# Kernel tuning notes

Hardware: AMD Instinct MI355X
Metric: run time of the kernel (lower is better)

## Reference

```python
import jax, jax.numpy as jnp
import numpy as np

B, S, HID, NH, NKV, HD, PS = 4, 1024, 4096, 32, 8, 128, 16
PPS = S // PS            # pages per sequence
NP = B * PPS             # total pages
NNZ = B * S


def _llama31_freqs(head_dim):
    # flashinfer apply_llama31_rope defaults: theta=5e5, scale=8, low=1, high=4, old_ctx=8192
    half = head_dim // 2
    theta, scale, low_ff, high_ff, old_ctx = 500000.0, 8.0, 1.0, 4.0, 8192.0
    freq = 1.0 / (theta ** (jnp.arange(half, dtype=jnp.float32) * 2.0 / head_dim))
    wavelen = 2.0 * jnp.pi / freq
    low_wl, high_wl = old_ctx / low_ff, old_ctx / high_ff
    smooth = (old_ctx / wavelen - low_ff) / (high_ff - low_ff)
    return jnp.where(wavelen < high_wl, freq,
                     jnp.where(wavelen > low_wl, freq / scale,
                               (1.0 - smooth) * freq / scale + smooth * freq))


def _rope(x, pos, freqs):
    # x: [nnz, H, D], non-interleaved (rotate-half) layout
    ang = pos.astype(jnp.float32)[:, None] * freqs[None, :]          # [nnz, D/2]
    cos, sin = jnp.cos(ang)[:, None, :], jnp.sin(ang)[:, None, :]    # [nnz, 1, D/2]
    x1, x2 = jnp.split(x, 2, axis=-1)
    return jnp.concatenate([x1 * cos - x2 * sin, x2 * cos + x1 * sin], axis=-1)


def setup_inputs() -> dict:
    key = jax.random.key(0)
    ks = jax.random.split(key, 6)
    std = 0.02
    return {
        "hidden_states": jax.random.normal(ks[0], (NNZ, HID), jnp.float32),
        "wq": jax.random.normal(ks[1], (NH * HD, HID), jnp.float32) * std,
        "wk": jax.random.normal(ks[2], (NKV * HD, HID), jnp.float32) * std,
        "wv": jax.random.normal(ks[3], (NKV * HD, HID), jnp.float32) * std,
        "wo": jax.random.normal(ks[4], (HID, NH * HD), jnp.float32) * std,
        "kv_cache": jnp.zeros((1, NP, 2, PS, NKV, HD), jnp.float32),
        "position_ids": jnp.tile(jnp.arange(S, dtype=jnp.int32), B),
        "kv_page_indices": jnp.arange(NP, dtype=jnp.int32),
        "kv_page_indptr": jnp.arange(B + 1, dtype=jnp.int32) * PPS,
        "kv_last_page_lens": jnp.full((B,), PS, jnp.int32),
        "qo_indptr": jnp.arange(B + 1, dtype=jnp.int32) * S,
    }


def reference(hidden_states, wq, wk, wv, wo, kv_cache, position_ids,
              kv_page_indices, kv_page_indptr, kv_last_page_lens, qo_indptr):
    nnz = hidden_states.shape[0]
    b = qo_indptr.shape[0] - 1
    s = nnz // b
    # fused QKV projections (nn.Linear stores [out, in])
    q = (hidden_states @ wq.T).reshape(nnz, NH, HD)
    k = (hidden_states @ wk.T).reshape(nnz, NKV, HD)
    v = (hidden_states @ wv.T).reshape(nnz, NKV, HD)
    # inline Llama-3.1 RoPE with per-token position ids
    freqs = _llama31_freqs(HD)
    q = _rope(q, position_ids, freqs)
    k = _rope(k, position_ids, freqs)
    # paged-KV append: scatter k/v into pages at (page_id, slot)
    cache = kv_cache[0]                                   # [NP, 2, PS, NKV, HD]
    ps = cache.shape[2]
    pages = kv_page_indices.reshape(b, -1)                # [B, PPS]
    bidx = jnp.repeat(jnp.arange(b), s)
    pid = pages[bidx, position_ids // ps]
    slot = position_ids % ps
    cache = cache.at[pid, 0, slot].set(k).at[pid, 1, slot].set(v)
    # paged attention: gather per-sequence K/V from pages, causal SDPA with GQA
    flat = pages.reshape(-1)
    kf = cache[flat, 0].reshape(b, s, NKV, HD)
    vf = cache[flat, 1].reshape(b, s, NKV, HD)
    g = NH // NKV
    kr = jnp.repeat(kf, g, axis=2)                        # [B, S, NH, HD]
    vr = jnp.repeat(vf, g, axis=2)
    qb = q.reshape(b, s, NH, HD)
    scale = 1.0 / jnp.sqrt(jnp.float32(HD))
    scores = jnp.einsum('bqhd,bkhd->bhqk', qb, kr) * scale
    mask = jnp.tril(jnp.ones((s, s), bool))
    scores = jnp.where(mask[None, None], scores, jnp.float32(-1e30))
    attn = jax.nn.softmax(scores, axis=-1)
    out = jnp.einsum('bhqk,bkhd->bqhd', attn, vr).reshape(nnz, NH * HD)
    return out @ wo.T
```

## Files before the change

kernel.cpp:

```cpp
#include <hip/hip_runtime.h>

typedef unsigned short u16;
typedef __bf16 bf16x8 __attribute__((ext_vector_type(8)));
typedef float f32x4 __attribute__((ext_vector_type(4)));

__device__ __forceinline__ u16 f2bf(float f) {
  unsigned int u = __float_as_uint(f);
  u += 0x7fffu + ((u >> 16) & 1u);
  return (u16)(u >> 16);
}
__device__ __forceinline__ float bf2f(u16 v) {
  return __uint_as_float(((unsigned int)v) << 16);
}

__device__ __forceinline__ void gl_lds16(const u16* g, u16* l) {
  auto* lp = reinterpret_cast<__attribute__((address_space(3))) unsigned int*>(
      reinterpret_cast<uintptr_t>(l));
  auto* gp = reinterpret_cast<const __attribute__((address_space(1))) unsigned int*>(
      reinterpret_cast<uintptr_t>(g));
  __builtin_amdgcn_global_load_lds(gp, lp, 16, 0, 0);
}

__global__ __launch_bounds__(256) void cvt_kernel(const float* __restrict__ in,
                                                  u16* __restrict__ out, int n4) {
  int i = blockIdx.x * 256 + threadIdx.x;
  if (i >= n4) return;
  float4 v = ((const float4*)in)[i];
  ushort4 o;
  o.x = f2bf(v.x); o.y = f2bf(v.y); o.z = f2bf(v.z); o.w = f2bf(v.w);
  ((ushort4*)out)[i] = o;
}

template <int OUT_BF16>
__global__ __launch_bounds__(256) void gemm_bt(const u16* __restrict__ A,
                                               const u16* __restrict__ B,
                                               void* __restrict__ Cv, int M, int N, int K) {
  __shared__ u16 As[128 * 32];
  __shared__ u16 Bs[128 * 32];
  const int t = threadIdx.x;
  const int lane = t & 63, w = t >> 6;
  const int col = lane & 15, quad = lane >> 4;
  const int m0 = blockIdx.y * 128, n0 = blockIdx.x * 128;

  f32x4 acc[4][4] = {};

  const int r4 = t >> 2;
  const int c8 = (t & 3) * 8;
  const u16* gA0 = A + (size_t)(m0 + r4) * K + c8;
  const u16* gA1 = A + (size_t)(m0 + 64 + r4) * K + c8;
  const u16* gB0 = B + (size_t)(n0 + r4) * K + c8;
  const u16* gB1 = B + (size_t)(n0 + 64 + r4) * K + c8;
  u16* lA0 = As + w * 512;
  u16* lA1 = As + 2048 + w * 512;
  u16* lB0 = Bs + w * 512;
  u16* lB1 = Bs + 2048 + w * 512;

  const int mr = (w & 1) * 64, nr = (w >> 1) * 64;

  for (int k0 = 0; k0 < K; k0 += 32) {
    __syncthreads();
    gl_lds16(gA0 + k0, lA0);
    gl_lds16(gA1 + k0, lA1);
    gl_lds16(gB0 + k0, lB0);
    gl_lds16(gB1 + k0, lB1);
    __syncthreads();

    bf16x8 a[4], b[4];
#pragma unroll
    for (int i = 0; i < 4; i++)
      a[i] = *(const bf16x8*)&As[(mr + i * 16 + col) * 32 + quad * 8];
#pragma unroll
    for (int i = 0; i < 4; i++)
      b[i] = *(const bf16x8*)&Bs[(nr + i * 16 + col) * 32 + quad * 8];
#pragma unroll
    for (int i = 0; i < 4; i++)
#pragma unroll
      for (int j = 0; j < 4; j++)
        acc[i][j] = __builtin_amdgcn_mfma_f32_16x16x32_bf16(a[i], b[j], acc[i][j], 0, 0, 0);
  }

#pragma unroll
  for (int i = 0; i < 4; i++) {
#pragma unroll
    for (int j = 0; j < 4; j++) {
      int mb = m0 + mr + i * 16 + quad * 4;
      int n = n0 + nr + j * 16 + col;
#pragma unroll
      for (int r = 0; r < 4; r++) {
        float v = acc[i][j][r];
        if constexpr (OUT_BF16)
          ((u16*)Cv)[(size_t)(mb + r) * N + n] = f2bf(v);
        else
          ((float*)Cv)[(size_t)(mb + r) * N + n] = v;
      }
    }
  }
}

__global__ __launch_bounds__(256) void transpose_kernel(const u16* __restrict__ in,
                                                        u16* __restrict__ out,
                                                        int in_stride, int out_stride) {
  __shared__ u16 tile[64][72];
  const int t = threadIdx.x;
  const int bm = blockIdx.y;
  const int bn = blockIdx.x;
  const int r = t >> 3, c = (t & 7) * 8;
  const u16* src = in + (size_t)(bm * 64 + r) * in_stride + bn * 64 + c;
  *(uint4*)&tile[r][c] = *(const uint4*)src;
  *(uint4*)&tile[r + 32][c] = *(const uint4*)(src + (size_t)32 * in_stride);
  __syncthreads();
  u16 vals[8];
  u16* dst = out + (size_t)(bn * 64 + r) * out_stride + bm * 64 + c;
#pragma unroll
  for (int i = 0; i < 8; i++) vals[i] = tile[c + i][r];
  *(uint4*)dst = *(uint4*)vals;
#pragma unroll
  for (int i = 0; i < 8; i++) vals[i] = tile[c + i][r + 32];
  *(uint4*)(dst + (size_t)32 * out_stride) = *(uint4*)vals;
}

__global__ __launch_bounds__(256) void rope_kernel(u16* __restrict__ X,
                                                   const int* __restrict__ pos_ids,
                                                   int log2H, int row_stride) {
  int tid = blockIdx.x * 256 + threadIdx.x;
  int i = tid & 63;
  int rest = tid >> 6;
  int h = rest & ((1 << log2H) - 1);
  int token = rest >> log2H;
  float pos = (float)pos_ids[token];
  float fr = __builtin_exp2f(-(float)i * (18.93156856932417f / 64.0f));
  float wl = 6.283185307179586f / fr;
  float f2;
  if (wl < 2048.0f) f2 = fr;
  else if (wl > 8192.0f) f2 = fr * 0.125f;
  else {
    float sm = (8192.0f / wl - 1.0f) * (1.0f / 3.0f);
    f2 = (1.0f - sm) * fr * 0.125f + sm * fr;
  }
  float ang = pos * f2;
  float ss = sinf(ang), cc = cosf(ang);
  size_t base = (size_t)token * row_stride + (size_t)h * 128 + i;
  float x1 = bf2f(X[base]), x2 = bf2f(X[base + 64]);
  X[base] = f2bf(x1 * cc - x2 * ss);
  X[base + 64] = f2bf(x2 * cc + x1 * ss);
}

__global__ __launch_bounds__(256) void attn_kernel(const u16* __restrict__ Qg,
                                                   const u16* __restrict__ Kg,
                                                   const u16* __restrict__ VTg,
                                                   u16* __restrict__ Og,
                                                   int QS, int KS) {
  const int qt = 15 - blockIdx.x;
  const int h = blockIdx.y, b = blockIdx.z;
  const int kvh = h >> 2;
  const int t = threadIdx.x, lane = t & 63, w = t >> 6;
  const int col = lane & 15, quad = lane >> 4;

  __shared__ u16 Ks[64 * 128];
  __shared__ u16 Vt[128 * 64];
  __shared__ u16 Ps[4][16][72];

  {
    const u16* Qbase = Qg + (size_t)(b * 1024 + qt * 64) * QS + h * 128;
#pragma unroll
    for (int c = 0; c < 4; c++) {
      int ch = w * 4 + c;
      int row = ch * 4 + (lane >> 4);
      int g = (lane & 15) ^ (row & 15);
      gl_lds16(Qbase + (size_t)row * QS + g * 8, Ks + ch * 512);
    }
  }
  __syncthreads();
  bf16x8 qa[4];
#pragma unroll
  for (int kk = 0; kk < 4; kk++) {
    int row = w * 16 + col;
    qa[kk] = *(const bf16x8*)&Ks[row * 128 + (((quad + 4 * kk) ^ col) << 3)];
  }

  f32x4 o[8] = {};
  float m_i[4] = {-3.0e38f, -3.0e38f, -3.0e38f, -3.0e38f};
  float l_i[4] = {};

  const float cf = 0.08838834764831845f * 1.4426950408889634f;
  const int qrow0 = qt * 64 + w * 16 + quad * 4;

  const u16* Kbase = Kg + (size_t)(b * 1024) * KS + kvh * 128;
  const u16* Vbase = VTg + (size_t)(kvh * 128) * 4096 + b * 1024;

  for (int j = 0; j <= qt; j++) {
    __syncthreads();
#pragma unroll
    for (int c = 0; c < 4; c++) {
      int ch = w * 4 + c;
      int krow = ch * 4 + (lane >> 4);
      int kg = (lane & 15) ^ (krow & 15);
      gl_lds16(Kbase + (size_t)(j * 64 + krow) * KS + kg * 8, Ks + ch * 512);
      int vrow = ch * 8 + (lane >> 3);
      int vg = (lane & 7) ^ (vrow & 7);
      gl_lds16(Vbase + (size_t)vrow * 4096 + j * 64 + vg * 8, Vt + ch * 512);
    }
    __syncthreads();

    f32x4 s[4] = {};
#pragma unroll
    for (int nb = 0; nb < 4; nb++) {
      int key = nb * 16 + col;
#pragma unroll
      for (int kk = 0; kk < 4; kk++) {
        bf16x8 kb2 = *(const bf16x8*)&Ks[key * 128 + (((quad + 4 * kk) ^ col) << 3)];
        s[nb] = __builtin_amdgcn_mfma_f32_16x16x32_bf16(qa[kk], kb2, s[nb], 0, 0, 0);
      }
    }

    if (j == qt) {
#pragma unroll
      for (int nb = 0; nb < 4; nb++)
#pragma unroll
        for (int rr = 0; rr < 4; rr++)
          if (j * 64 + nb * 16 + col > qrow0 + rr) s[nb][rr] = -3.0e38f;
    }

    float mnew[4];
#pragma unroll
    for (int rr = 0; rr < 4; rr++) {
      mnew[rr] = m_i[rr];
#pragma unroll
      for (int nb = 0; nb < 4; nb++) mnew[rr] = fmaxf(mnew[rr], s[nb][rr]);
    }
#pragma unroll
    for (int off = 1; off < 16; off <<= 1)
#pragma unroll
      for (int rr = 0; rr < 4; rr++)
        mnew[rr] = fmaxf(mnew[rr], __shfl_xor(mnew[rr], off));

    float p[4][4], rs[4], alpha[4];
#pragma unroll
    for (int rr = 0; rr < 4; rr++) {
      alpha[rr] = __builtin_exp2f((m_i[rr] - mnew[rr]) * cf);
      m_i[rr] = mnew[rr];
      rs[rr] = 0.0f;
    }
#pragma unroll
    for (int nb = 0; nb < 4; nb++)
#pragma unroll
      for (int rr = 0; rr < 4; rr++) {
        p[nb][rr] = __builtin_exp2f((s[nb][rr] - mnew[rr]) * cf);
        rs[rr] += p[nb][rr];
      }
#pragma unroll
    for (int off = 1; off < 16; off <<= 1)
#pragma unroll
      for (int rr = 0; rr < 4; rr++) rs[rr] += __shfl_xor(rs[rr], off);
#pragma unroll
    for (int rr = 0; rr < 4; rr++) l_i[rr] = l_i[rr] * alpha[rr] + rs[rr];
#pragma unroll
    for (int nb2 = 0; nb2 < 8; nb2++)
#pragma unroll
      for (int rr = 0; rr < 4; rr++) o[nb2][rr] *= alpha[rr];

#pragma unroll
    for (int nb = 0; nb < 4; nb++)
#pragma unroll
      for (int rr = 0; rr < 4; rr++)
        Ps[w][quad * 4 + rr][nb * 16 + col] = f2bf(p[nb][rr]);

    bf16x8 pa0 = *(const bf16x8*)&Ps[w][col][quad * 8];
    bf16x8 pa1 = *(const bf16x8*)&Ps[w][col][quad * 8 + 32];
#pragma unroll
    for (int nb2 = 0; nb2 < 8; nb2++) {
      int d = nb2 * 16 + col;
      bf16x8 vb0 = *(const bf16x8*)&Vt[d * 64 + ((quad ^ (col & 7)) << 3)];
      bf16x8 vb1 = *(const bf16x8*)&Vt[d * 64 + ((((quad + 4) & 7) ^ (col & 7)) << 3)];
      o[nb2] = __builtin_amdgcn_mfma_f32_16x16x32_bf16(pa0, vb0, o[nb2], 0, 0, 0);
      o[nb2] = __builtin_amdgcn_mfma_f32_16x16x32_bf16(pa1, vb1, o[nb2], 0, 0, 0);
    }
  }

  float inv[4];
#pragma unroll
  for (int rr = 0; rr < 4; rr++) inv[rr] = 1.0f / l_i[rr];
#pragma unroll
  for (int nb2 = 0; nb2 < 8; nb2++)
#pragma unroll
    for (int rr = 0; rr < 4; rr++) {
      size_t off2 = (size_t)(b * 1024 + qt * 64 + w * 16 + quad * 4 + rr) * 4096 +
                    h * 128 + nb2 * 16 + col;
      Og[off2] = f2bf(o[nb2][rr] * inv[rr]);
    }
}

extern "C" void kernel_launch(void* const* d_in, const int* in_sizes, int n_in,
                              void* d_out, int out_size, void* d_ws, size_t ws_size,
                              hipStream_t stream) {
  const float* hs = (const float*)d_in[0];
  const float* wq = (const float*)d_in[1];
  const float* wk = (const float*)d_in[2];
  const float* wv = (const float*)d_in[3];
  const float* wo = (const float*)d_in[4];
  const int* pos = (const int*)d_in[6];
  float* out = (float*)d_out;

  char* ws = (char*)d_ws;
  const size_t MB = 1ull << 20;
  u16* hs_bf   = (u16*)(ws + 0);
  u16* wqkv_bf = (u16*)(ws + 32 * MB);
  u16* QKV     = (u16*)(ws + 80 * MB);
  u16* wo_bf = (u16*)(ws + 0);
  u16* AOb   = (u16*)(ws + 32 * MB);
  u16* VTb   = (u16*)(ws + 64 * MB);

  cvt_kernel<<<16384, 256, 0, stream>>>(hs, hs_bf, 4194304);
  cvt_kernel<<<16384, 256, 0, stream>>>(wq, wqkv_bf, 4194304);
  cvt_kernel<<<4096, 256, 0, stream>>>(wk, wqkv_bf + 16777216, 1048576);
  cvt_kernel<<<4096, 256, 0, stream>>>(wv, wqkv_bf + 20971520, 1048576);

  gemm_bt<1><<<dim3(48, 32), 256, 0, stream>>>(hs_bf, wqkv_bf, QKV, 4096, 6144, 4096);

  rope_kernel<<<32768, 256, 0, stream>>>(QKV, pos, 5, 6144);
  rope_kernel<<<8192, 256, 0, stream>>>(QKV + 4096, pos, 3, 6144);

  transpose_kernel<<<dim3(16, 64), 256, 0, stream>>>(QKV + 5120, VTb, 6144, 4096);

  cvt_kernel<<<16384, 256, 0, stream>>>(wo, wo_bf, 4194304);

  attn_kernel<<<dim3(16, 32, 4), 256, 0, stream>>>(QKV, QKV + 4096, VTb, AOb, 6144, 6144);

  gemm_bt<0><<<dim3(32, 32), 256, 0, stream>>>(AOb, wo_bf, out, 4096, 4096, 4096);
}
```

Measured before the change: 890.6 us.

## Replace GEMM with 256x256 double-buffered 8-wave pipelined kernel

Replaces the simple 128x128 single-buffered bf16 GEMM, which synchronises twice per K step, with a 256x256-tile, 512-thread kernel. The new kernel double-buffers LDS and interleaves global-to-LDS staging with MFMA quadrants under fine-grained barriers and vmcnt waits. It also adds an XOR swizzle on LDS to avoid bank conflicts, XCD-aware block remapping for L2 locality, and raised MFMA priority via setprio. The larger tiles raise reuse per load but cut the block count (384 and 256 blocks), and the hand-scheduled barrier sequence is fragile.

```diff
diff --git a/kernel.cpp b/kernel.cpp
--- a/kernel.cpp
+++ b/kernel.cpp
@@ -31,60 +31,139 @@
   ((ushort4*)out)[i] = o;
 }
 
+
+#define BARRIER() __builtin_amdgcn_s_barrier()
+#define VMCNT(n_) asm volatile("s_waitcnt vmcnt(" #n_ ")" ::: "memory")
+#define PH_SYNC()                                           \
+  do {                                                      \
+    BARRIER();                                              \
+    asm volatile("s_waitcnt lgkmcnt(0)" ::: "memory");      \
+    __builtin_amdgcn_sched_barrier(0);                      \
+  } while (0)
+
+#define STAGE_A(b_, h_, kt_)                                                        \
+  gl_lds16(gA + (size_t)((h_) * 128) * K + (size_t)(kt_) * 32,                      \
+           lds + (b_) * 16384 + (h_) * 4096 + w * 512)
+
+#define STAGE_B(b_, h_, kt_)                                                        \
+  gl_lds16(gB + (size_t)((h_) * 128) * K + (size_t)(kt_) * 32,                      \
+           lds + (b_) * 16384 + 8192 + (h_) * 4096 + w * 512)
+
+#define LOADS_A(b_, qm_)                                                            \
+  do {                                                                              \
+    _Pragma("unroll") for (int i2 = 0; i2 < 4; i2++)                                \
+      ar[i2] = *(const bf16x8*)&lds[(b_) * 16384 + arow + ((qm_)*4 + i2) * 512 + ax]; \
+  } while (0)
+
+#define LOADS_B(b_, qn_)                                                            \
+  do {                                                                              \
+    _Pragma("unroll") for (int j2 = 0; j2 < 2; j2++)                                \
+      br[(qn_)*2 + j2] =                                                            \
+          *(const bf16x8*)&lds[(b_) * 16384 + brow + ((qn_)*2 + j2) * 512 + ax];    \
+  } while (0)
+
+#define MFMA_Q(qm_, qn_)                                                            \
+  do {                                                                              \
+    __builtin_amdgcn_s_setprio(1);                                                  \
+    _Pragma("unroll") for (int i2 = 0; i2 < 4; i2++) {                              \
+      _Pragma("unroll") for (int j2 = 0; j2 < 2; j2++) {                            \
+        acc[(qm_)*4 + i2][(qn_)*2 + j2] = __builtin_amdgcn_mfma_f32_16x16x32_bf16(  \
+            ar[i2], br[(qn_)*2 + j2], acc[(qm_)*4 + i2][(qn_)*2 + j2], 0, 0, 0);    \
+      }                                                                             \
+    }                                                                               \
+    __builtin_amdgcn_s_setprio(0);                                                  \
+  } while (0)
+
 template <int OUT_BF16>
-__global__ __launch_bounds__(256) void gemm_bt(const u16* __restrict__ A,
-                                               const u16* __restrict__ B,
-                                               void* __restrict__ Cv, int M, int N, int K) {
-  __shared__ u16 As[128 * 32];
-  __shared__ u16 Bs[128 * 32];
-  const int t = threadIdx.x;
-  const int lane = t & 63, w = t >> 6;
+__global__ __launch_bounds__(512, 2) void gemm8p(const u16* __restrict__ A,
+                                                 const u16* __restrict__ B,
+                                                 void* __restrict__ Cv,
+                                                 int M, int N, int K) {
+  __shared__ u16 lds[32768];
+  (void)M;
+  const int t = threadIdx.x, lane = t & 63, w = t >> 6;
   const int col = lane & 15, quad = lane >> 4;
-  const int m0 = blockIdx.y * 128, n0 = blockIdx.x * 128;
-
-  f32x4 acc[4][4] = {};
-
-  const int r4 = t >> 2;
-  const int c8 = (t & 3) * 8;
-  const u16* gA0 = A + (size_t)(m0 + r4) * K + c8;
-  const u16* gA1 = A + (size_t)(m0 + 64 + r4) * K + c8;
-  const u16* gB0 = B + (size_t)(n0 + r4) * K + c8;
-  const u16* gB1 = B + (size_t)(n0 + 64 + r4) * K + c8;
-  u16* lA0 = As + w * 512;
-  u16* lA1 = As + 2048 + w * 512;
-  u16* lB0 = Bs + w * 512;
-  u16* lB1 = Bs + 2048 + w * 512;
-
-  const int mr = (w & 1) * 64, nr = (w >> 1) * 64;
-
-  for (int k0 = 0; k0 < K; k0 += 32) {
-    __syncthreads();
-    gl_lds16(gA0 + k0, lA0);
-    gl_lds16(gA1 + k0, lA1);
-    gl_lds16(gB0 + k0, lB0);
-    gl_lds16(gB1 + k0, lB1);
-    __syncthreads();
-
-    bf16x8 a[4], b[4];
-#pragma unroll
-    for (int i = 0; i < 4; i++)
-      a[i] = *(const bf16x8*)&As[(mr + i * 16 + col) * 32 + quad * 8];
-#pragma unroll
-    for (int i = 0; i < 4; i++)
-      b[i] = *(const bf16x8*)&Bs[(nr + i * 16 + col) * 32 + quad * 8];
-#pragma unroll
-    for (int i = 0; i < 4; i++)
-#pragma unroll
-      for (int j = 0; j < 4; j++)
-        acc[i][j] = __builtin_amdgcn_mfma_f32_16x16x32_bf16(a[i], b[j], acc[i][j], 0, 0, 0);
-  }
-
-#pragma unroll
-  for (int i = 0; i < 4; i++) {
+  const int wm = w >> 2, wn = w & 3;
+
+  const int nwg = gridDim.x * gridDim.y;
+  const int wgid = blockIdx.y * gridDim.x + blockIdx.x;
+  const int xcd = wgid & 7, lin = wgid >> 3;
+  const int q8 = nwg >> 3, r8 = nwg & 7;
+  const int nid = (xcd < r8 ? xcd * (q8 + 1) : r8 * (q8 + 1) + (xcd - r8) * q8) + lin;
+  const int m0 = (nid / gridDim.x) * 256;
+  const int n0 = (nid % gridDim.x) * 256;
+
+  const int srow = t >> 2;
+  const int sj = (t & 3) ^ (srow & 3);
+  const u16* gA = A + (size_t)(m0 + srow) * K + sj * 8;
+  const u16* gB = B + (size_t)(n0 + srow) * K + sj * 8;
+
+  const int arow = (wm * 128 + col) * 32;
+  const int brow = 8192 + (wn * 64 + col) * 32;
+  const int ax = ((quad ^ (col & 3)) << 3);
+
+  f32x4 acc[8][4] = {};
+  bf16x8 ar[4], br[4];
+
+  STAGE_A(0, 0, 0); STAGE_A(0, 1, 0);
+  STAGE_B(0, 0, 0); STAGE_B(0, 1, 0);
+  STAGE_B(1, 0, 1); STAGE_B(1, 1, 1);
+  VMCNT(2);
+  BARRIER();
+
+  const int NIT = K >> 6;
+  for (int it = 0; it < NIT - 1; ++it) {
+    const int kt = it * 2;
+    LOADS_A(0, 0); LOADS_B(0, 0);
+    STAGE_A(1, 0, kt + 1);
+    PH_SYNC(); MFMA_Q(0, 0); BARRIER();
+    LOADS_B(0, 1);
+    STAGE_A(1, 1, kt + 1);
+    PH_SYNC(); MFMA_Q(0, 1); BARRIER();
+    LOADS_A(0, 1);
+    STAGE_B(0, 0, kt + 2);
+    PH_SYNC(); MFMA_Q(1, 0); BARRIER();
+    STAGE_B(0, 1, kt + 2);
+    PH_SYNC(); MFMA_Q(1, 1); VMCNT(2); BARRIER();
+    LOADS_A(1, 0); LOADS_B(1, 0);
+    STAGE_A(0, 0, kt + 2);
+    PH_SYNC(); MFMA_Q(0, 0); BARRIER();
+    LOADS_B(1, 1);
+    STAGE_A(0, 1, kt + 2);
+    PH_SYNC(); MFMA_Q(0, 1); BARRIER();
+    LOADS_A(1, 1);
+    STAGE_B(1, 0, kt + 3);
+    PH_SYNC(); MFMA_Q(1, 0); BARRIER();
+    STAGE_B(1, 1, kt + 3);
+    PH_SYNC(); MFMA_Q(1, 1); VMCNT(2); BARRIER();
+  }
+
+  {
+    const int kl = 2 * NIT - 1;
+    LOADS_A(0, 0); LOADS_B(0, 0);
+    STAGE_A(1, 0, kl);
+    PH_SYNC(); MFMA_Q(0, 0); BARRIER();
+    LOADS_B(0, 1);
+    STAGE_A(1, 1, kl);
+    PH_SYNC(); MFMA_Q(0, 1); BARRIER();
+    LOADS_A(0, 1);
+    PH_SYNC(); MFMA_Q(1, 0); BARRIER();
+    PH_SYNC(); MFMA_Q(1, 1); VMCNT(0); BARRIER();
+    LOADS_A(1, 0); LOADS_B(1, 0);
+    PH_SYNC(); MFMA_Q(0, 0); BARRIER();
+    LOADS_B(1, 1);
+    PH_SYNC(); MFMA_Q(0, 1); BARRIER();
+    LOADS_A(1, 1);
+    PH_SYNC(); MFMA_Q(1, 0); BARRIER();
+    MFMA_Q(1, 1);
+  }
+
+#pragma unroll
+  for (int i = 0; i < 8; i++) {
 #pragma unroll
     for (int j = 0; j < 4; j++) {
-      int mb = m0 + mr + i * 16 + quad * 4;
-      int n = n0 + nr + j * 16 + col;
+      const int mb = m0 + wm * 128 + i * 16 + quad * 4;
+      const int n = n0 + wn * 64 + j * 16 + col;
 #pragma unroll
       for (int r = 0; r < 4; r++) {
         float v = acc[i][j][r];
@@ -315,7 +394,7 @@
   cvt_kernel<<<4096, 256, 0, stream>>>(wk, wqkv_bf + 16777216, 1048576);
   cvt_kernel<<<4096, 256, 0, stream>>>(wv, wqkv_bf + 20971520, 1048576);
 
-  gemm_bt<1><<<dim3(48, 32), 256, 0, stream>>>(hs_bf, wqkv_bf, QKV, 4096, 6144, 4096);
+  gemm8p<1><<<dim3(24, 16), 512, 0, stream>>>(hs_bf, wqkv_bf, QKV, 4096, 6144, 4096);
 
   rope_kernel<<<32768, 256, 0, stream>>>(QKV, pos, 5, 6144);
   rope_kernel<<<8192, 256, 0, stream>>>(QKV + 4096, pos, 3, 6144);
@@ -326,5 +405,5 @@
 
   attn_kernel<<<dim3(16, 32, 4), 256, 0, stream>>>(QKV, QKV + 4096, VTb, AOb, 6144, 6144);
 
-  gemm_bt<0><<<dim3(32, 32), 256, 0, stream>>>(AOb, wo_bf, out, 4096, 4096, 4096);
-}
+  gemm8p<0><<<dim3(16, 16), 512, 0, stream>>>(AOb, wo_bf, out, 4096, 4096, 4096);
+}
```

New measurement: 823.0 us. -7.6%, faster.
